# Kernel optimization log

Hardware: AMD Instinct MI355X
Metric: run time of the kernel (lower is better)

Reference implementation:

```python
import jax, jax.numpy as jnp
import numpy as np

N = 100000   # nodes
E = 1600000  # edges per view
B = 256      # graphs in batch
D = 128      # feature dim
H, C = 4, 32 # heads, per-head channels (H*C = 128)


def _seg_softmax(logits, seg, num_seg):
    # numerically stable softmax over segments (per-destination / per-graph)
    m = jax.ops.segment_max(logits, seg, num_segments=num_seg)
    e = jnp.exp(logits - m[seg])
    s = jax.ops.segment_sum(e, seg, num_segments=num_seg)
    return e / s[seg]


def _gat_conv(x, edge_index, W, att_src, att_dst, bias):
    # PyG GATConv with add_self_loops=True, concat heads
    n = x.shape[0]
    loop = jnp.arange(n, dtype=edge_index.dtype)
    src = jnp.concatenate([edge_index[0], loop])
    dst = jnp.concatenate([edge_index[1], loop])
    xh = (x @ W).reshape(n, H, C)                      # [N,H,C]
    a_src = jnp.einsum('nhc,hc->nh', xh, att_src)      # [N,H]
    a_dst = jnp.einsum('nhc,hc->nh', xh, att_dst)
    alpha = jax.nn.leaky_relu(a_src[src] + a_dst[dst], 0.2)   # [E+N,H]
    alpha = _seg_softmax(alpha, dst, n)
    msg = xh[src] * alpha[..., None]                   # [E+N,H,C]
    out = jax.ops.segment_sum(msg, dst, num_segments=n)
    return out.reshape(n, H * C) + bias


def _global_attention(h, batch, gate_W, gate_b):
    gate = (h @ gate_W + gate_b)[:, 0]                 # [N]
    a = _seg_softmax(gate, batch, B)
    return jax.ops.segment_sum(a[:, None] * h, batch, num_segments=B)  # [B,128]


def setup_inputs() -> dict:
    key = jax.random.key(0)
    ks = jax.random.split(key, 32)
    p = lambda k, shp: (jax.random.normal(k, shp, dtype=jnp.float32) * 0.05)
    inp = {
        'x': jax.random.normal(ks[0], (N, D), dtype=jnp.float32),
        'edge_index_ast': jax.random.randint(ks[1], (2, E), 0, N, dtype=jnp.int32),
        'edge_index_cfg': jax.random.randint(ks[2], (2, E), 0, N, dtype=jnp.int32),
        'edge_index_pdg': jax.random.randint(ks[3], (2, E), 0, N, dtype=jnp.int32),
        'batch': jnp.sort(jax.random.randint(ks[4], (N,), 0, B, dtype=jnp.int32)),
        'ln_g': jnp.ones((D,), jnp.float32),
        'ln_b': jnp.zeros((D,), jnp.float32),
        'proj_W': p(ks[5], (D, D)), 'proj_b': p(ks[6], (D,)),
        'W_ast': p(ks[7], (D, H * C)), 'att_src_ast': p(ks[8], (H, C)), 'att_dst_ast': p(ks[9], (H, C)), 'bias_ast': p(ks[10], (H * C,)),
        'W_cfg': p(ks[11], (D, H * C)), 'att_src_cfg': p(ks[12], (H, C)), 'att_dst_cfg': p(ks[13], (H, C)), 'bias_cfg': p(ks[14], (H * C,)),
        'W_pdg': p(ks[15], (D, H * C)), 'att_src_pdg': p(ks[16], (H, C)), 'att_dst_pdg': p(ks[17], (H, C)), 'bias_pdg': p(ks[18], (H * C,)),
        'gate_W': p(ks[19], (H * C, 1)), 'gate_b': p(ks[20], (1,)),
        'clf_W1': p(ks[21], (3 * H * C, 128)), 'clf_b1': p(ks[22], (128,)),
        'clf_W2': p(ks[23], (128, 1)), 'clf_b2': p(ks[24], (1,)),
    }
    return inp


def reference(x, edge_index_ast, edge_index_cfg, edge_index_pdg, batch,
              ln_g, ln_b, proj_W, proj_b,
              W_ast, att_src_ast, att_dst_ast, bias_ast,
              W_cfg, att_src_cfg, att_dst_cfg, bias_cfg,
              W_pdg, att_src_pdg, att_dst_pdg, bias_pdg,
              gate_W, gate_b, clf_W1, clf_b1, clf_W2, clf_b2):
    # LayerNorm + proj + LeakyReLU (dropout = eval/no-op)
    mu = jnp.mean(x, axis=-1, keepdims=True)
    var = jnp.var(x, axis=-1, keepdims=True)
    xn = (x - mu) * jax.lax.rsqrt(var + 1e-5) * ln_g + ln_b
    h0 = jax.nn.leaky_relu(xn @ proj_W + proj_b, 0.01)

    h_ast = jax.nn.elu(_gat_conv(h0, edge_index_ast, W_ast, att_src_ast, att_dst_ast, bias_ast))
    g_ast = _global_attention(h_ast, batch, gate_W, gate_b)
    h_cfg = jax.nn.elu(_gat_conv(h0, edge_index_cfg, W_cfg, att_src_cfg, att_dst_cfg, bias_cfg))
    g_cfg = _global_attention(h_cfg, batch, gate_W, gate_b)
    h_pdg = jax.nn.elu(_gat_conv(h0, edge_index_pdg, W_pdg, att_src_pdg, att_dst_pdg, bias_pdg))
    g_pdg = _global_attention(h_pdg, batch, gate_W, gate_b)

    combined = jnp.concatenate([g_ast, g_cfg, g_pdg], axis=1)  # [B, 384]
    hid = jax.nn.leaky_relu(combined @ clf_W1 + clf_b1, 0.01)
    return (hid @ clf_W2 + clf_b2).reshape(-1)                 # [B]
```

## Files before the change

kernel.cpp:

```cpp
#include <hip/hip_runtime.h>
#include <hip/hip_bf16.h>
#include <hip/hip_fp16.h>
#include <math.h>

#define NN 100000
#define EE 1600000
#define BB 256
#define DD 128
#define NBUCK 391
#define PBLK 384
#define CH 4167
#define TOTB (3 * PBLK)
#define ROWS_PAD 100096
#define EPV (EE + NN)

typedef short bf16x8 __attribute__((ext_vector_type(8)));
typedef float f32x4 __attribute__((ext_vector_type(4)));

__device__ __forceinline__ float bf2f(unsigned short u) {
    return __uint_as_float(((unsigned int)u) << 16);
}
__device__ __forceinline__ unsigned short f2bf(float f) {
    __hip_bfloat16 h = __float2bfloat16(f);
    return *(unsigned short*)&h;
}
__device__ __forceinline__ unsigned short f2h(float f) {
    __half h = __float2half(f);
    return *(unsigned short*)&h;
}
__device__ __forceinline__ float h2f(unsigned short u) {
    __half h = *(__half*)&u;
    return __half2float(h);
}

__global__ __launch_bounds__(256) void pack_wt(const float* __restrict__ W0,
                                               const float* __restrict__ W1,
                                               const float* __restrict__ W2,
                                               const float* __restrict__ W3,
                                               const float* __restrict__ ln_g,
                                               unsigned short* __restrict__ WT) {
    int which = blockIdx.y;
    const float* W = which == 0 ? W0 : which == 1 ? W1 : which == 2 ? W2 : W3;
    int i = blockIdx.x * 256 + threadIdx.x;
    int n = i >> 7, k = i & 127;
    float v = W[k * 128 + n];
    if (which == 0) v *= ln_g[k];
    WT[which * 16384 + i] = f2bf(v);
}

__global__ __launch_bounds__(128) void ln_consts(const float* __restrict__ W,
                                                 const float* __restrict__ g,
                                                 const float* __restrict__ b,
                                                 float* __restrict__ c12) {
    int n = threadIdx.x;
    float c1 = 0.f, c2 = 0.f;
    for (int k = 0; k < 128; k++) {
        float w = W[k * 128 + n];
        c1 = fmaf(g[k], w, c1);
        c2 = fmaf(b[k], w, c2);
    }
    c12[n] = c1;
    c12[128 + n] = c2;
}

__global__ __launch_bounds__(256) void gemm_proj(const float* __restrict__ X,
                                                 const unsigned short* __restrict__ WT,
                                                 const float* __restrict__ c12,
                                                 const float* __restrict__ pb,
                                                 unsigned short* __restrict__ Out) {
    int w = threadIdx.x >> 6, lane = threadIdx.x & 63;
    int ln = lane & 15, oct = lane >> 4;
    int row0 = blockIdx.x * 128 + w * 32;

    f32x4 acc[2][8];
    #pragma unroll
    for (int i = 0; i < 2; i++)
        #pragma unroll
        for (int j = 0; j < 8; j++) acc[i][j] = (f32x4){0.f, 0.f, 0.f, 0.f};

    const float* X0 = X + (size_t)(row0 + ln) * 128;
    const float* X1 = X + (size_t)(row0 + 16 + ln) * 128;
    const bf16x8* Wr = (const bf16x8*)(WT + (size_t)ln * 128);

    float s0 = 0.f, q0 = 0.f, s1 = 0.f, q1 = 0.f;
    #pragma unroll
    for (int kq = 0; kq < 4; kq++) {
        int koff = kq * 4 + oct;
        float4 xa = *(const float4*)(X0 + koff * 8);
        float4 xb = *(const float4*)(X0 + koff * 8 + 4);
        float4 ya = *(const float4*)(X1 + koff * 8);
        float4 yb = *(const float4*)(X1 + koff * 8 + 4);
        s0 += (xa.x + xa.y) + (xa.z + xa.w) + (xb.x + xb.y) + (xb.z + xb.w);
        q0 += xa.x * xa.x + xa.y * xa.y + xa.z * xa.z + xa.w * xa.w
            + xb.x * xb.x + xb.y * xb.y + xb.z * xb.z + xb.w * xb.w;
        s1 += (ya.x + ya.y) + (ya.z + ya.w) + (yb.x + yb.y) + (yb.z + yb.w);
        q1 += ya.x * ya.x + ya.y * ya.y + ya.z * ya.z + ya.w * ya.w
            + yb.x * yb.x + yb.y * yb.y + yb.z * yb.z + yb.w * yb.w;
        bf16x8 a0, a1;
        a0[0] = (short)f2bf(xa.x); a0[1] = (short)f2bf(xa.y); a0[2] = (short)f2bf(xa.z); a0[3] = (short)f2bf(xa.w);
        a0[4] = (short)f2bf(xb.x); a0[5] = (short)f2bf(xb.y); a0[6] = (short)f2bf(xb.z); a0[7] = (short)f2bf(xb.w);
        a1[0] = (short)f2bf(ya.x); a1[1] = (short)f2bf(ya.y); a1[2] = (short)f2bf(ya.z); a1[3] = (short)f2bf(ya.w);
        a1[4] = (short)f2bf(yb.x); a1[5] = (short)f2bf(yb.y); a1[6] = (short)f2bf(yb.z); a1[7] = (short)f2bf(yb.w);
        #pragma unroll
        for (int ct = 0; ct < 8; ct++) {
            bf16x8 bfr = Wr[ct * 16 * 16 + koff];
            acc[0][ct] = __builtin_amdgcn_mfma_f32_16x16x32_bf16(a0, bfr, acc[0][ct], 0, 0, 0);
            acc[1][ct] = __builtin_amdgcn_mfma_f32_16x16x32_bf16(a1, bfr, acc[1][ct], 0, 0, 0);
        }
    }
    #pragma unroll
    for (int m = 16; m < 64; m <<= 1) {
        s0 += __shfl_xor(s0, m); q0 += __shfl_xor(q0, m);
        s1 += __shfl_xor(s1, m); q1 += __shfl_xor(q1, m);
    }
    float mu0 = s0 * (1.0f / 128.0f);
    float rs0 = rsqrtf(q0 * (1.0f / 128.0f) - mu0 * mu0 + 1e-5f);
    float mu1 = s1 * (1.0f / 128.0f);
    float rs1 = rsqrtf(q1 * (1.0f / 128.0f) - mu1 * mu1 + 1e-5f);

    float c1v[8], c2v[8], pbv[8];
    #pragma unroll
    for (int ct = 0; ct < 8; ct++) {
        c1v[ct] = c12[ct * 16 + ln];
        c2v[ct] = c12[128 + ct * 16 + ln];
        pbv[ct] = pb[ct * 16 + ln];
    }

    #pragma unroll
    for (int rt = 0; rt < 2; rt++) {
        #pragma unroll
        for (int r = 0; r < 4; r++) {
            int src = oct * 4 + r;
            float rs_r = __shfl(rt ? rs1 : rs0, src);
            float mu_r = __shfl(rt ? mu1 : mu0, src);
            int row = row0 + rt * 16 + oct * 4 + r;
            #pragma unroll
            for (int ct = 0; ct < 8; ct++) {
                float v = rs_r * acc[rt][ct][r] - rs_r * mu_r * c1v[ct] + c2v[ct] + pbv[ct];
                v = v > 0.f ? v : 0.01f * v;
                Out[(size_t)row * 128 + ct * 16 + ln] = f2bf(v);
            }
        }
    }
}

__global__ __launch_bounds__(256) void gemm_view(const unsigned short* __restrict__ A,
                                                 const unsigned short* __restrict__ WT,
                                                 unsigned short* __restrict__ Out,
                                                 const float* __restrict__ asw,
                                                 const float* __restrict__ adw,
                                                 float* __restrict__ a_src,
                                                 float* __restrict__ a_dst) {
    int w = threadIdx.x >> 6, lane = threadIdx.x & 63;
    int ln = lane & 15, oct = lane >> 4;
    int row0 = blockIdx.x * 128 + w * 32;

    f32x4 acc[2][8];
    #pragma unroll
    for (int i = 0; i < 2; i++)
        #pragma unroll
        for (int j = 0; j < 8; j++) acc[i][j] = (f32x4){0.f, 0.f, 0.f, 0.f};

    const bf16x8* Ar0 = (const bf16x8*)(A + (size_t)(row0 + ln) * 128);
    const bf16x8* Ar1 = (const bf16x8*)(A + (size_t)(row0 + 16 + ln) * 128);
    const bf16x8* Wr  = (const bf16x8*)(WT + (size_t)ln * 128);

    #pragma unroll
    for (int kq = 0; kq < 4; kq++) {
        int koff = kq * 4 + oct;
        bf16x8 a0 = Ar0[koff];
        bf16x8 a1 = Ar1[koff];
        #pragma unroll
        for (int ct = 0; ct < 8; ct++) {
            bf16x8 bfr = Wr[ct * 16 * 16 + koff];
            acc[0][ct] = __builtin_amdgcn_mfma_f32_16x16x32_bf16(a0, bfr, acc[0][ct], 0, 0, 0);
            acc[1][ct] = __builtin_amdgcn_mfma_f32_16x16x32_bf16(a1, bfr, acc[1][ct], 0, 0, 0);
        }
    }

    float aswv[8], adwv[8];
    #pragma unroll
    for (int ct = 0; ct < 8; ct++) { aswv[ct] = asw[ct * 16 + ln]; adwv[ct] = adw[ct * 16 + ln]; }

    #pragma unroll
    for (int rt = 0; rt < 2; rt++) {
        #pragma unroll
        for (int r = 0; r < 4; r++) {
            int row = row0 + rt * 16 + oct * 4 + r;
            float sh_[4] = {0.f, 0.f, 0.f, 0.f}, dh_[4] = {0.f, 0.f, 0.f, 0.f};
            #pragma unroll
            for (int ct = 0; ct < 8; ct++) {
                float v = acc[rt][ct][r];
                Out[(size_t)row * 128 + ct * 16 + ln] = f2bf(v);
                sh_[ct >> 1] = fmaf(v, aswv[ct], sh_[ct >> 1]);
                dh_[ct >> 1] = fmaf(v, adwv[ct], dh_[ct >> 1]);
            }
            #pragma unroll
            for (int off = 1; off < 16; off <<= 1) {
                #pragma unroll
                for (int h = 0; h < 4; h++) {
                    sh_[h] += __shfl_xor(sh_[h], off);
                    dh_[h] += __shfl_xor(dh_[h], off);
                }
            }
            if (ln == 0) {
                *(float4*)(a_src + (size_t)row * 4) = make_float4(sh_[0], sh_[1], sh_[2], sh_[3]);
                *(float4*)(a_dst + (size_t)row * 4) = make_float4(dh_[0], dh_[1], dh_[2], dh_[3]);
            }
        }
    }
}

__global__ __launch_bounds__(256) void csr_hist(const int* __restrict__ e0,
                                                const int* __restrict__ e1,
                                                const int* __restrict__ e2,
                                                int* __restrict__ blockHistT) {
    int v = blockIdx.x / PBLK, p = blockIdx.x % PBLK;
    const int* ei = v == 0 ? e0 : v == 1 ? e1 : e2;
    __shared__ int h[NBUCK];
    for (int i = threadIdx.x; i < NBUCK; i += 256) h[i] = 0;
    __syncthreads();
    int ea = p * CH, ebnd = min(EE, ea + CH);
    int e = ea + threadIdx.x;
    for (; e + 768 < ebnd; e += 1024) {
        int d0 = ei[EE + e], d1 = ei[EE + e + 256];
        int d2 = ei[EE + e + 512], d3 = ei[EE + e + 768];
        atomicAdd(&h[((unsigned)d0) >> 8], 1);
        atomicAdd(&h[((unsigned)d1) >> 8], 1);
        atomicAdd(&h[((unsigned)d2) >> 8], 1);
        atomicAdd(&h[((unsigned)d3) >> 8], 1);
    }
    for (; e < ebnd; e += 256) atomicAdd(&h[((unsigned)ei[EE + e]) >> 8], 1);
    __syncthreads();
    for (int i = threadIdx.x; i < NBUCK; i += 256) blockHistT[i * TOTB + blockIdx.x] = h[i];
}

__global__ __launch_bounds__(256) void csr_bsum(const int* __restrict__ blockHistT,
                                                int* __restrict__ btot) {
    int wid = (blockIdx.x * 256 + threadIdx.x) >> 6;
    int lane = threadIdx.x & 63;
    if (wid >= 3 * NBUCK) return;
    int v = wid / NBUCK, b = wid - v * NBUCK;
    const int* row = blockHistT + (size_t)b * TOTB + v * PBLK;
    int s = 0;
    #pragma unroll
    for (int j = 0; j < 6; j++) s += row[lane * 6 + j];
    #pragma unroll
    for (int m = 1; m < 64; m <<= 1) s += __shfl_xor(s, m);
    if (lane == 0) btot[wid] = s;
}

__global__ __launch_bounds__(512) void csr_scan(const int* __restrict__ btot,
                                                int* __restrict__ ebstart,
                                                int* __restrict__ bstart) {
    int v = blockIdx.x, t = threadIdx.x;
    __shared__ int se[512], ss[512];
    int tot_e = (t < NBUCK) ? btot[v * NBUCK + t] : 0;
    int nval = (t < NBUCK) ? min(256, NN - t * 256) : 0;
    int tot_s = tot_e + nval;
    se[t] = tot_e; ss[t] = tot_s;
    __syncthreads();
    for (int s = 1; s < 512; s <<= 1) {
        int ae = (t >= s) ? se[t - s] : 0;
        int as_ = (t >= s) ? ss[t - s] : 0;
        __syncthreads();
        se[t] += ae; ss[t] += as_;
        __syncthreads();
    }
    if (t < NBUCK) {
        ebstart[v * (NBUCK + 1) + t] = se[t] - tot_e;
        bstart[v * (NBUCK + 1) + t] = ss[t] - tot_s;
    }
    if (t == NBUCK - 1) {
        ebstart[v * (NBUCK + 1) + NBUCK] = se[t];
        bstart[v * (NBUCK + 1) + NBUCK] = ss[t];
    }
}

__global__ __launch_bounds__(256) void csr_boff(const int* __restrict__ blockHistT,
                                                const int* __restrict__ ebstart,
                                                int* __restrict__ blockOffT) {
    int wid = (blockIdx.x * 256 + threadIdx.x) >> 6;
    int lane = threadIdx.x & 63;
    if (wid >= 3 * NBUCK) return;
    int v = wid / NBUCK, b = wid - v * NBUCK;
    const int* row = blockHistT + (size_t)b * TOTB + v * PBLK;
    int* orow = blockOffT + (size_t)b * TOTB + v * PBLK;
    int vals[6], lexcl[6];
    int ls = 0;
    #pragma unroll
    for (int j = 0; j < 6; j++) vals[j] = row[lane * 6 + j];
    #pragma unroll
    for (int j = 0; j < 6; j++) { lexcl[j] = ls; ls += vals[j]; }
    int incl = ls;
    #pragma unroll
    for (int m = 1; m < 64; m <<= 1) {
        int t = __shfl_up(incl, m);
        if (lane >= m) incl += t;
    }
    int wexcl = incl - ls;
    int base = ebstart[v * (NBUCK + 1) + b];
    #pragma unroll
    for (int j = 0; j < 6; j++) orow[lane * 6 + j] = base + wexcl + lexcl[j];
}

__global__ __launch_bounds__(256) void csr_scatter(const int* __restrict__ e0,
                                                   const int* __restrict__ e1,
                                                   const int* __restrict__ e2,
                                                   const int* __restrict__ blockOffT,
                                                   unsigned int* __restrict__ pairbuf) {
    int v = blockIdx.x / PBLK, p = blockIdx.x % PBLK;
    const int* ei = v == 0 ? e0 : v == 1 ? e1 : e2;
    __shared__ int cur[NBUCK];
    for (int i = threadIdx.x; i < NBUCK; i += 256) cur[i] = blockOffT[(size_t)i * TOTB + blockIdx.x];
    __syncthreads();
    int ea = p * CH, ebnd = min(EE, ea + CH);
    unsigned int* pb = pairbuf + (size_t)v * EE;
    int e = ea + threadIdx.x;
    for (; e + 768 < ebnd; e += 1024) {
        unsigned s0 = (unsigned)ei[e],       d0 = (unsigned)ei[EE + e];
        unsigned s1 = (unsigned)ei[e + 256], d1 = (unsigned)ei[EE + e + 256];
        unsigned s2 = (unsigned)ei[e + 512], d2 = (unsigned)ei[EE + e + 512];
        unsigned s3 = (unsigned)ei[e + 768], d3 = (unsigned)ei[EE + e + 768];
        int p0 = atomicAdd(&cur[d0 >> 8], 1);
        int p1 = atomicAdd(&cur[d1 >> 8], 1);
        int p2 = atomicAdd(&cur[d2 >> 8], 1);
        int p3 = atomicAdd(&cur[d3 >> 8], 1);
        pb[p0] = (s0 << 8) | (d0 & 255u);
        pb[p1] = (s1 << 8) | (d1 & 255u);
        pb[p2] = (s2 << 8) | (d2 & 255u);
        pb[p3] = (s3 << 8) | (d3 & 255u);
    }
    for (; e < ebnd; e += 256) {
        unsigned s = (unsigned)ei[e], d = (unsigned)ei[EE + e];
        int pos = atomicAdd(&cur[d >> 8], 1);
        pb[pos] = (s << 8) | (d & 255u);
    }
}

__global__ __launch_bounds__(256) void csr_fine(const unsigned int* __restrict__ pairbuf,
                                                const int* __restrict__ btot,
                                                const int* __restrict__ ebstart,
                                                const int* __restrict__ bstart,
                                                int* __restrict__ deg3,
                                                int* __restrict__ start3,
                                                unsigned int* __restrict__ ebuf3) {
    int v = blockIdx.x / NBUCK, b = blockIdx.x - v * NBUCK;
    int cnt   = btot[v * NBUCK + b];
    int pbase = ebstart[v * (NBUCK + 1) + b];
    int obase = bstart[v * (NBUCK + 1) + b];
    const unsigned int* pb = pairbuf + (size_t)v * EE + pbase;
    unsigned int* eb = ebuf3 + (size_t)v * EPV + obase;
    __shared__ int hist[256], scan[256], cur[256];
    int t = threadIdx.x;
    int node = b * 256 + t;
    int valid = (node < NN) ? 1 : 0;
    hist[t] = valid;
    __syncthreads();
    {
        int i = t;
        for (; i + 768 < cnt; i += 1024) {
            unsigned v0 = pb[i], v1 = pb[i + 256], v2 = pb[i + 512], v3 = pb[i + 768];
            atomicAdd(&hist[v0 & 255u], 1);
            atomicAdd(&hist[v1 & 255u], 1);
            atomicAdd(&hist[v2 & 255u], 1);
            atomicAdd(&hist[v3 & 255u], 1);
        }
        for (; i < cnt; i += 256) atomicAdd(&hist[pb[i] & 255u], 1);
    }
    __syncthreads();
    scan[t] = hist[t];
    __syncthreads();
    for (int s = 1; s < 256; s <<= 1) {
        int u = (t >= s) ? scan[t - s] : 0;
        __syncthreads();
        scan[t] += u;
        __syncthreads();
    }
    int excl = scan[t] - hist[t];
    cur[t] = excl + valid;
    if (valid) eb[excl] = (((unsigned)node) << 8) | ((unsigned)node & 255u);
    __syncthreads();
    {
        int i = t;
        for (; i + 768 < cnt; i += 1024) {
            unsigned v0 = pb[i], v1 = pb[i + 256], v2 = pb[i + 512], v3 = pb[i + 768];
            int p0 = atomicAdd(&cur[v0 & 255u], 1);
            int p1 = atomicAdd(&cur[v1 & 255u], 1);
            int p2 = atomicAdd(&cur[v2 & 255u], 1);
            int p3 = atomicAdd(&cur[v3 & 255u], 1);
            eb[p0] = v0; eb[p1] = v1; eb[p2] = v2; eb[p3] = v3;
        }
        for (; i < cnt; i += 256) {
            unsigned int val = pb[i];
            int pos = atomicAdd(&cur[val & 255u], 1);
            eb[pos] = val;
        }
    }
    if (valid) {
        deg3[v * NN + node] = hist[t];
        start3[v * NN + node] = obase + excl;
    }
}

__global__ __launch_bounds__(256) void aggregate_kernel(const unsigned short* __restrict__ xh,
                                                        const int* __restrict__ start,
                                                        const int* __restrict__ deg,
                                                        const unsigned int* __restrict__ ebuf,
                                                        const float* __restrict__ a_src,
                                                        const float* __restrict__ a_dst,
                                                        const float* __restrict__ bias,
                                                        const float* __restrict__ gw,
                                                        const float* __restrict__ gb,
                                                        unsigned short* __restrict__ hvb,
                                                        float* __restrict__ gexpv) {
    int node = (blockIdx.x * 256 + threadIdx.x) >> 6;
    int lane = threadIdx.x & 63;
    if (node >= NN) return;
    int h = lane >> 4;
    int st = start[node];
    int cnt = deg[node];
    const char* xb = (const char*)xh;
    int laneoff = lane * 4;
    float4 ad4 = *(const float4*)(a_dst + (size_t)node * 4);

    float accx = 0.f, accy = 0.f, den = 0.f;
    for (int j0 = 0; j0 < cnt; j0 += 64) {
        int nj = min(64, cnt - j0);
        int src_l = 0;
        unsigned u01 = 0, u23 = 0;
        if (lane < nj) {
            src_l = (int)(ebuf[st + j0 + lane] >> 8);
            float4 as4 = *(const float4*)(a_src + (size_t)src_l * 4);
            float t0 = as4.x + ad4.x, t1 = as4.y + ad4.y;
            float t2 = as4.z + ad4.z, t3 = as4.w + ad4.w;
            t0 = fmaxf(t0, 0.f) + 0.2f * fminf(t0, 0.f);
            t1 = fmaxf(t1, 0.f) + 0.2f * fminf(t1, 0.f);
            t2 = fmaxf(t2, 0.f) + 0.2f * fminf(t2, 0.f);
            t3 = fmaxf(t3, 0.f) + 0.2f * fminf(t3, 0.f);
            u01 = (unsigned)f2h(exp2f(t0 * 1.442695041f)) |
                  ((unsigned)f2h(exp2f(t1 * 1.442695041f)) << 16);
            u23 = (unsigned)f2h(exp2f(t2 * 1.442695041f)) |
                  ((unsigned)f2h(exp2f(t3 * 1.442695041f)) << 16);
        }
        int jj = 0;
        for (; jj + 4 <= nj; jj += 4) {
            int s0 = __builtin_amdgcn_readlane(src_l, jj);
            int s1 = __builtin_amdgcn_readlane(src_l, jj + 1);
            int s2 = __builtin_amdgcn_readlane(src_l, jj + 2);
            int s3 = __builtin_amdgcn_readlane(src_l, jj + 3);
            unsigned pa0 = (unsigned)__builtin_amdgcn_readlane((int)u01, jj);
            unsigned pb0 = (unsigned)__builtin_amdgcn_readlane((int)u23, jj);
            unsigned pa1 = (unsigned)__builtin_amdgcn_readlane((int)u01, jj + 1);
            unsigned pb1 = (unsigned)__builtin_amdgcn_readlane((int)u23, jj + 1);
            unsigned pa2 = (unsigned)__builtin_amdgcn_readlane((int)u01, jj + 2);
            unsigned pb2 = (unsigned)__builtin_amdgcn_readlane((int)u23, jj + 2);
            unsigned pa3 = (unsigned)__builtin_amdgcn_readlane((int)u01, jj + 3);
            unsigned pb3 = (unsigned)__builtin_amdgcn_readlane((int)u23, jj + 3);
            unsigned k0 = (h < 2) ? pa0 : pb0;
            unsigned k1 = (h < 2) ? pa1 : pb1;
            unsigned k2 = (h < 2) ? pa2 : pb2;
            unsigned k3 = (h < 2) ? pa3 : pb3;
            float w0 = h2f((unsigned short)((h & 1) ? (k0 >> 16) : (k0 & 0xffffu)));
            float w1 = h2f((unsigned short)((h & 1) ? (k1 >> 16) : (k1 & 0xffffu)));
            float w2 = h2f((unsigned short)((h & 1) ? (k2 >> 16) : (k2 & 0xffffu)));
            float w3 = h2f((unsigned short)((h & 1) ? (k3 >> 16) : (k3 & 0xffffu)));
            unsigned int x0 = *(const unsigned int*)(xb + (((size_t)(unsigned)s0) << 8) + laneoff);
            unsigned int x1 = *(const unsigned int*)(xb + (((size_t)(unsigned)s1) << 8) + laneoff);
            unsigned int x2 = *(const unsigned int*)(xb + (((size_t)(unsigned)s2) << 8) + laneoff);
            unsigned int x3 = *(const unsigned int*)(xb + (((size_t)(unsigned)s3) << 8) + laneoff);
            den += (w0 + w1) + (w2 + w3);
            accx = fmaf(w0, __uint_as_float(x0 << 16), accx);
            accy = fmaf(w0, __uint_as_float(x0 & 0xffff0000u), accy);
            accx = fmaf(w1, __uint_as_float(x1 << 16), accx);
            accy = fmaf(w1, __uint_as_float(x1 & 0xffff0000u), accy);
            accx = fmaf(w2, __uint_as_float(x2 << 16), accx);
            accy = fmaf(w2, __uint_as_float(x2 & 0xffff0000u), accy);
            accx = fmaf(w3, __uint_as_float(x3 << 16), accx);
            accy = fmaf(w3, __uint_as_float(x3 & 0xffff0000u), accy);
        }
        for (; jj < nj; jj++) {
            int s = __builtin_amdgcn_readlane(src_l, jj);
            unsigned pa = (unsigned)__builtin_amdgcn_readlane((int)u01, jj);
            unsigned pbk = (unsigned)__builtin_amdgcn_readlane((int)u23, jj);
            unsigned k = (h < 2) ? pa : pbk;
            float w = h2f((unsigned short)((h & 1) ? (k >> 16) : (k & 0xffffu)));
            unsigned int xv = *(const unsigned int*)(xb + (((size_t)(unsigned)s) << 8) + laneoff);
            den += w;
            accx = fmaf(w, __uint_as_float(xv << 16), accx);
            accy = fmaf(w, __uint_as_float(xv & 0xffff0000u), accy);
        }
    }
    float inv = 1.0f / den;
    float2 bb = *(const float2*)(bias + lane * 2);
    float o0 = accx * inv + bb.x;
    float o1 = accy * inv + bb.y;
    o0 = o0 > 0.f ? o0 : exp2f(o0 * 1.442695041f) - 1.0f;
    o1 = o1 > 0.f ? o1 : exp2f(o1 * 1.442695041f) - 1.0f;
    unsigned int packed = (unsigned)f2bf(o0) | ((unsigned)f2bf(o1) << 16);
    *(unsigned int*)(hvb + (size_t)node * 128 + lane * 2) = packed;
    float2 g2 = *(const float2*)(gw + lane * 2);
    float gp = o0 * g2.x + o1 * g2.y;
    #pragma unroll
    for (int m = 1; m < 64; m <<= 1) gp += __shfl_xor(gp, m);
    if (lane == 0) gexpv[node] = exp2f((gp + gb[0]) * 1.442695041f);
}

__global__ __launch_bounds__(1024) void pool_kernel(const unsigned short* __restrict__ hvb,
                                                    const float* __restrict__ gexpv,
                                                    const int* __restrict__ batch,
                                                    float* __restrict__ gout,
                                                    int voff) {
    int b = blockIdx.x;
    int g = threadIdx.x >> 7;
    int ch = threadIdx.x & 127;
    int l = 0, r = NN;
    while (l < r) { int m = (l + r) >> 1; if (batch[m] < b) l = m + 1; else r = m; }
    int s0 = l;
    r = NN;
    while (l < r) { int m = (l + r) >> 1; if (batch[m] < b + 1) l = m + 1; else r = m; }
    int s1 = l;
    float acc = 0.f, wsum = 0.f;
    for (int n = s0 + g; n < s1; n += 8) {
        float w = gexpv[n];
        wsum += w;
        acc = fmaf(w, bf2f(hvb[(size_t)n * 128 + ch]), acc);
    }
    __shared__ float sacc[8][128];
    __shared__ float sws[8];
    sacc[g][ch] = acc;
    if (ch == 0) sws[g] = wsum;
    __syncthreads();
    if (g == 0) {
        float a = 0.f, w = 0.f;
        #pragma unroll
        for (int i = 0; i < 8; i++) { a += sacc[i][ch]; w += sws[i]; }
        gout[b * 384 + voff + ch] = (s1 > s0) ? a / w : 0.f;
    }
}

__global__ __launch_bounds__(128) void clf_kernel(const float* __restrict__ gout,
                                                  const float* __restrict__ W1,
                                                  const float* __restrict__ b1,
                                                  const float* __restrict__ W2,
                                                  const float* __restrict__ b2,
                                                  float* __restrict__ out) {
    int b = blockIdx.x;
    int j = threadIdx.x;
    float acc = b1[j];
    for (int k = 0; k < 384; k++) acc = fmaf(gout[b * 384 + k], W1[k * 128 + j], acc);
    acc = acc > 0.f ? acc : 0.01f * acc;
    float p = acc * W2[j];
    #pragma unroll
    for (int m = 1; m < 64; m <<= 1) p += __shfl_xor(p, m);
    __shared__ float sh[2];
    if ((j & 63) == 0) sh[j >> 6] = p;
    __syncthreads();
    if (j == 0) out[b] = sh[0] + sh[1] + b2[0];
}

extern "C" void kernel_launch(void* const* d_in, const int* in_sizes, int n_in,
                              void* d_out, int out_size, void* d_ws, size_t ws_size,
                              hipStream_t stream) {
    const float* x      = (const float*)d_in[0];
    const int*   ei[3]  = {(const int*)d_in[1], (const int*)d_in[2], (const int*)d_in[3]};
    const int*   batch  = (const int*)d_in[4];
    const float* ln_g   = (const float*)d_in[5];
    const float* ln_b   = (const float*)d_in[6];
    const float* proj_W = (const float*)d_in[7];
    const float* proj_b = (const float*)d_in[8];
    const float* Wv[3]  = {(const float*)d_in[9],  (const float*)d_in[13], (const float*)d_in[17]};
    const float* asv[3] = {(const float*)d_in[10], (const float*)d_in[14], (const float*)d_in[18]};
    const float* adv[3] = {(const float*)d_in[11], (const float*)d_in[15], (const float*)d_in[19]};
    const float* bv[3]  = {(const float*)d_in[12], (const float*)d_in[16], (const float*)d_in[20]};
    const float* gate_W = (const float*)d_in[21];
    const float* gate_b = (const float*)d_in[22];
    const float* clf_W1 = (const float*)d_in[23];
    const float* clf_b1 = (const float*)d_in[24];
    const float* clf_W2 = (const float*)d_in[25];
    const float* clf_b2 = (const float*)d_in[26];
    float* out = (float*)d_out;

    (void)in_sizes; (void)n_in; (void)out_size; (void)ws_size;

    char* base = (char*)d_ws;
    size_t off = 0;
    auto nxt = [&](size_t bytes) { char* r = base + off; off += (bytes + 255) & ~(size_t)255; return r; };
    unsigned short* h0   = (unsigned short*)nxt((size_t)ROWS_PAD * 128 * 2);
    unsigned short* xh   = (unsigned short*)nxt((size_t)ROWS_PAD * 128 * 2);
    unsigned short* hvb  = (unsigned short*)nxt((size_t)NN * 128 * 2);
    unsigned short* WT   = (unsigned short*)nxt(4 * 16384 * 2);
    float* c12    = (float*)nxt(256 * 4);
    float* a_src  = (float*)nxt((size_t)ROWS_PAD * 4 * 4);
    float* a_dst  = (float*)nxt((size_t)ROWS_PAD * 4 * 4);
    float* gexpv  = (float*)nxt(NN * 4);
    float* gout   = (float*)nxt(BB * 384 * 4);
    int* deg3     = (int*)nxt(3 * NN * 4);
    int* start3   = (int*)nxt(3 * NN * 4);
    unsigned int* ebuf3 = (unsigned int*)nxt(((size_t)3 * EPV + 64) * 4);
    int* btot     = (int*)nxt(3 * NBUCK * 4);
    int* ebstart  = (int*)nxt(3 * (NBUCK + 1) * 4);
    int* bstart   = (int*)nxt(3 * (NBUCK + 1) * 4);
    int* blockHistT = (int*)nxt((size_t)NBUCK * TOTB * 4);
    int* blockOffT  = (int*)nxt((size_t)NBUCK * TOTB * 4);
    unsigned int* pairbuf = (unsigned int*)nxt((size_t)3 * EE * 4);

    pack_wt<<<dim3(64, 4), 256, 0, stream>>>(proj_W, Wv[0], Wv[1], Wv[2], ln_g, WT);
    ln_consts<<<1, 128, 0, stream>>>(proj_W, ln_g, ln_b, c12);
    csr_hist<<<TOTB, 256, 0, stream>>>(ei[0], ei[1], ei[2], blockHistT);
    csr_bsum<<<(3 * NBUCK + 3) / 4, 256, 0, stream>>>(blockHistT, btot);
    csr_scan<<<3, 512, 0, stream>>>(btot, ebstart, bstart);
    csr_boff<<<(3 * NBUCK + 3) / 4, 256, 0, stream>>>(blockHistT, ebstart, blockOffT);
    csr_scatter<<<TOTB, 256, 0, stream>>>(ei[0], ei[1], ei[2], blockOffT, pairbuf);
    csr_fine<<<3 * NBUCK, 256, 0, stream>>>(pairbuf, btot, ebstart, bstart, deg3, start3, ebuf3);
    gemm_proj<<<782, 256, 0, stream>>>(x, WT, c12, proj_b, h0);
    for (int v = 0; v < 3; v++) {
        gemm_view<<<782, 256, 0, stream>>>(h0, WT + (1 + v) * 16384, xh,
                                           asv[v], adv[v], a_src, a_dst);
        aggregate_kernel<<<25000, 256, 0, stream>>>(xh, start3 + v * NN, deg3 + v * NN,
                                                    ebuf3 + (size_t)v * EPV,
                                                    a_src, a_dst,
                                                    bv[v], gate_W, gate_b, hvb, gexpv);
        pool_kernel<<<256, 1024, 0, stream>>>(hvb, gexpv, batch, gout, v * 128);
    }
    clf_kernel<<<256, 128, 0, stream>>>(gout, clf_W1, clf_b1, clf_W2, clf_b2, out);
}
```

Measured before the change: 710.2 us.

## Fuse CSR build kernels with projection GEMMs and switch features to fp16

```diff
diff --git a/kernel.cpp b/kernel.cpp
--- a/kernel.cpp
+++ b/kernel.cpp
@@ -6,20 +6,17 @@
 #define NN 100000
 #define EE 1600000
 #define BB 256
-#define DD 128
 #define NBUCK 391
 #define PBLK 384
 #define CH 4167
 #define TOTB (3 * PBLK)
 #define ROWS_PAD 100096
 #define EPV (EE + NN)
+#define LOG2E 1.442695041f
 
 typedef short bf16x8 __attribute__((ext_vector_type(8)));
 typedef float f32x4 __attribute__((ext_vector_type(4)));
 
-__device__ __forceinline__ float bf2f(unsigned short u) {
-    return __uint_as_float(((unsigned int)u) << 16);
-}
 __device__ __forceinline__ unsigned short f2bf(float f) {
     __hip_bfloat16 h = __float2bfloat16(f);
     return *(unsigned short*)&h;
@@ -63,14 +60,41 @@
     c12[128 + n] = c2;
 }
 
-__global__ __launch_bounds__(256) void gemm_proj(const float* __restrict__ X,
-                                                 const unsigned short* __restrict__ WT,
-                                                 const float* __restrict__ c12,
-                                                 const float* __restrict__ pb,
-                                                 unsigned short* __restrict__ Out) {
-    int w = threadIdx.x >> 6, lane = threadIdx.x & 63;
+
+__device__ __forceinline__ void hist_body(int bid, int tid,
+                                          const int* __restrict__ e0,
+                                          const int* __restrict__ e1,
+                                          const int* __restrict__ e2,
+                                          int* __restrict__ blockHistT) {
+    int v = bid / PBLK, p = bid % PBLK;
+    const int* ei = v == 0 ? e0 : v == 1 ? e1 : e2;
+    __shared__ int h[NBUCK];
+    for (int i = tid; i < NBUCK; i += 256) h[i] = 0;
+    __syncthreads();
+    int ea = p * CH, ebnd = min(EE, ea + CH);
+    int e = ea + tid;
+    for (; e + 768 < ebnd; e += 1024) {
+        int d0 = ei[EE + e], d1 = ei[EE + e + 256];
+        int d2 = ei[EE + e + 512], d3 = ei[EE + e + 768];
+        atomicAdd(&h[((unsigned)d0) >> 8], 1);
+        atomicAdd(&h[((unsigned)d1) >> 8], 1);
+        atomicAdd(&h[((unsigned)d2) >> 8], 1);
+        atomicAdd(&h[((unsigned)d3) >> 8], 1);
+    }
+    for (; e < ebnd; e += 256) atomicAdd(&h[((unsigned)ei[EE + e]) >> 8], 1);
+    __syncthreads();
+    for (int i = tid; i < NBUCK; i += 256) blockHistT[i * TOTB + bid] = h[i];
+}
+
+__device__ __forceinline__ void proj_body(int nb, int tid,
+                                          const float* __restrict__ X,
+                                          const unsigned short* __restrict__ WT,
+                                          const float* __restrict__ c12,
+                                          const float* __restrict__ pb,
+                                          unsigned short* __restrict__ Out) {
+    int w = tid >> 6, lane = tid & 63;
     int ln = lane & 15, oct = lane >> 4;
-    int row0 = blockIdx.x * 128 + w * 32;
+    int row0 = nb * 128 + w * 32;
 
     f32x4 acc[2][8];
     #pragma unroll
@@ -78,8 +102,8 @@
         #pragma unroll
         for (int j = 0; j < 8; j++) acc[i][j] = (f32x4){0.f, 0.f, 0.f, 0.f};
 
-    const float* X0 = X + (size_t)(row0 + ln) * 128;
-    const float* X1 = X + (size_t)(row0 + 16 + ln) * 128;
+    const float* X0 = X + (size_t)min(row0 + ln, NN - 1) * 128;
+    const float* X1 = X + (size_t)min(row0 + 16 + ln, NN - 1) * 128;
     const bf16x8* Wr = (const bf16x8*)(WT + (size_t)ln * 128);
 
     float s0 = 0.f, q0 = 0.f, s1 = 0.f, q1 = 0.f;
@@ -125,7 +149,6 @@
         c2v[ct] = c12[128 + ct * 16 + ln];
         pbv[ct] = pb[ct * 16 + ln];
     }
-
     #pragma unroll
     for (int rt = 0; rt < 2; rt++) {
         #pragma unroll
@@ -144,16 +167,52 @@
     }
 }
 
-__global__ __launch_bounds__(256) void gemm_view(const unsigned short* __restrict__ A,
-                                                 const unsigned short* __restrict__ WT,
-                                                 unsigned short* __restrict__ Out,
-                                                 const float* __restrict__ asw,
-                                                 const float* __restrict__ adw,
-                                                 float* __restrict__ a_src,
-                                                 float* __restrict__ a_dst) {
-    int w = threadIdx.x >> 6, lane = threadIdx.x & 63;
+__device__ __forceinline__ void scatter_body(int bid, int tid,
+                                             const int* __restrict__ e0,
+                                             const int* __restrict__ e1,
+                                             const int* __restrict__ e2,
+                                             const int* __restrict__ blockOffT,
+                                             unsigned int* __restrict__ pairbuf) {
+    int v = bid / PBLK, p = bid % PBLK;
+    const int* ei = v == 0 ? e0 : v == 1 ? e1 : e2;
+    __shared__ int cur[NBUCK];
+    for (int i = tid; i < NBUCK; i += 256) cur[i] = blockOffT[(size_t)i * TOTB + bid];
+    __syncthreads();
+    int ea = p * CH, ebnd = min(EE, ea + CH);
+    unsigned int* pbuf = pairbuf + (size_t)v * EE;
+    int e = ea + tid;
+    for (; e + 768 < ebnd; e += 1024) {
+        unsigned s0 = (unsigned)ei[e],       d0 = (unsigned)ei[EE + e];
+        unsigned s1 = (unsigned)ei[e + 256], d1 = (unsigned)ei[EE + e + 256];
+        unsigned s2 = (unsigned)ei[e + 512], d2 = (unsigned)ei[EE + e + 512];
+        unsigned s3 = (unsigned)ei[e + 768], d3 = (unsigned)ei[EE + e + 768];
+        int p0 = atomicAdd(&cur[d0 >> 8], 1);
+        int p1 = atomicAdd(&cur[d1 >> 8], 1);
+        int p2 = atomicAdd(&cur[d2 >> 8], 1);
+        int p3 = atomicAdd(&cur[d3 >> 8], 1);
+        pbuf[p0] = (s0 << 8) | (d0 & 255u);
+        pbuf[p1] = (s1 << 8) | (d1 & 255u);
+        pbuf[p2] = (s2 << 8) | (d2 & 255u);
+        pbuf[p3] = (s3 << 8) | (d3 & 255u);
+    }
+    for (; e < ebnd; e += 256) {
+        unsigned s = (unsigned)ei[e], d = (unsigned)ei[EE + e];
+        int pos = atomicAdd(&cur[d >> 8], 1);
+        pbuf[pos] = (s << 8) | (d & 255u);
+    }
+}
+
+__device__ __forceinline__ void view_body(int nb, int tid,
+                                          const unsigned short* __restrict__ h0,
+                                          const unsigned short* __restrict__ WTv,
+                                          const float* __restrict__ asw,
+                                          const float* __restrict__ adw,
+                                          unsigned short* __restrict__ Out,
+                                          float* __restrict__ a_src,
+                                          float* __restrict__ a_dst) {
+    int w = tid >> 6, lane = tid & 63;
     int ln = lane & 15, oct = lane >> 4;
-    int row0 = blockIdx.x * 128 + w * 32;
+    int row0 = nb * 128 + w * 32;
 
     f32x4 acc[2][8];
     #pragma unroll
@@ -161,9 +220,9 @@
         #pragma unroll
         for (int j = 0; j < 8; j++) acc[i][j] = (f32x4){0.f, 0.f, 0.f, 0.f};
 
-    const bf16x8* Ar0 = (const bf16x8*)(A + (size_t)(row0 + ln) * 128);
-    const bf16x8* Ar1 = (const bf16x8*)(A + (size_t)(row0 + 16 + ln) * 128);
-    const bf16x8* Wr  = (const bf16x8*)(WT + (size_t)ln * 128);
+    const bf16x8* Ar0 = (const bf16x8*)(h0 + (size_t)(row0 + ln) * 128);
+    const bf16x8* Ar1 = (const bf16x8*)(h0 + (size_t)(row0 + 16 + ln) * 128);
+    const bf16x8* Wr  = (const bf16x8*)(WTv + (size_t)ln * 128);
 
     #pragma unroll
     for (int kq = 0; kq < 4; kq++) {
@@ -177,7 +236,6 @@
             acc[1][ct] = __builtin_amdgcn_mfma_f32_16x16x32_bf16(a1, bfr, acc[1][ct], 0, 0, 0);
         }
     }
-
     float aswv[8], adwv[8];
     #pragma unroll
     for (int ct = 0; ct < 8; ct++) { aswv[ct] = asw[ct * 16 + ln]; adwv[ct] = adw[ct * 16 + ln]; }
@@ -190,10 +248,10 @@
             float sh_[4] = {0.f, 0.f, 0.f, 0.f}, dh_[4] = {0.f, 0.f, 0.f, 0.f};
             #pragma unroll
             for (int ct = 0; ct < 8; ct++) {
-                float v = acc[rt][ct][r];
-                Out[(size_t)row * 128 + ct * 16 + ln] = f2bf(v);
-                sh_[ct >> 1] = fmaf(v, aswv[ct], sh_[ct >> 1]);
-                dh_[ct >> 1] = fmaf(v, adwv[ct], dh_[ct >> 1]);
+                float vv = acc[rt][ct][r];
+                Out[(size_t)row * 128 + ct * 16 + ln] = f2h(vv);
+                sh_[ct >> 1] = fmaf(vv, aswv[ct], sh_[ct >> 1]);
+                dh_[ct >> 1] = fmaf(vv, adwv[ct], dh_[ct >> 1]);
             }
             #pragma unroll
             for (int off = 1; off < 16; off <<= 1) {
@@ -211,28 +269,32 @@
     }
 }
 
-__global__ __launch_bounds__(256) void csr_hist(const int* __restrict__ e0,
-                                                const int* __restrict__ e1,
-                                                const int* __restrict__ e2,
-                                                int* __restrict__ blockHistT) {
-    int v = blockIdx.x / PBLK, p = blockIdx.x % PBLK;
-    const int* ei = v == 0 ? e0 : v == 1 ? e1 : e2;
-    __shared__ int h[NBUCK];
-    for (int i = threadIdx.x; i < NBUCK; i += 256) h[i] = 0;
-    __syncthreads();
-    int ea = p * CH, ebnd = min(EE, ea + CH);
-    int e = ea + threadIdx.x;
-    for (; e + 768 < ebnd; e += 1024) {
-        int d0 = ei[EE + e], d1 = ei[EE + e + 256];
-        int d2 = ei[EE + e + 512], d3 = ei[EE + e + 768];
-        atomicAdd(&h[((unsigned)d0) >> 8], 1);
-        atomicAdd(&h[((unsigned)d1) >> 8], 1);
-        atomicAdd(&h[((unsigned)d2) >> 8], 1);
-        atomicAdd(&h[((unsigned)d3) >> 8], 1);
-    }
-    for (; e < ebnd; e += 256) atomicAdd(&h[((unsigned)ei[EE + e]) >> 8], 1);
-    __syncthreads();
-    for (int i = threadIdx.x; i < NBUCK; i += 256) blockHistT[i * TOTB + blockIdx.x] = h[i];
+__global__ __launch_bounds__(256) void fat_hist_proj(const int* e0, const int* e1, const int* e2,
+                                                     int* blockHistT,
+                                                     const float* X, const unsigned short* WT,
+                                                     const float* c12, const float* pb,
+                                                     unsigned short* h0) {
+    if (blockIdx.x < TOTB) hist_body(blockIdx.x, threadIdx.x, e0, e1, e2, blockHistT);
+    else proj_body(blockIdx.x - TOTB, threadIdx.x, X, WT, c12, pb, h0);
+}
+
+__global__ __launch_bounds__(256) void fat_scatter_view(const int* e0, const int* e1, const int* e2,
+                                                        const int* blockOffT, unsigned int* pairbuf,
+                                                        const unsigned short* h0, const unsigned short* WT,
+                                                        const float* as0, const float* ad0,
+                                                        unsigned short* xh, float* a_src, float* a_dst) {
+    if (blockIdx.x < TOTB) scatter_body(blockIdx.x, threadIdx.x, e0, e1, e2, blockOffT, pairbuf);
+    else view_body(blockIdx.x - TOTB, threadIdx.x, h0, WT + 16384, as0, ad0, xh, a_src, a_dst);
+}
+
+__global__ __launch_bounds__(256) void gemm_view(const unsigned short* __restrict__ h0,
+                                                 const unsigned short* __restrict__ WTv,
+                                                 const float* __restrict__ asw,
+                                                 const float* __restrict__ adw,
+                                                 unsigned short* __restrict__ Out,
+                                                 float* __restrict__ a_src,
+                                                 float* __restrict__ a_dst) {
+    view_body(blockIdx.x, threadIdx.x, h0, WTv, asw, adw, Out, a_src, a_dst);
 }
 
 __global__ __launch_bounds__(256) void csr_bsum(const int* __restrict__ blockHistT,
@@ -302,40 +364,6 @@
     int base = ebstart[v * (NBUCK + 1) + b];
     #pragma unroll
     for (int j = 0; j < 6; j++) orow[lane * 6 + j] = base + wexcl + lexcl[j];
-}
-
-__global__ __launch_bounds__(256) void csr_scatter(const int* __restrict__ e0,
-                                                   const int* __restrict__ e1,
-                                                   const int* __restrict__ e2,
-                                                   const int* __restrict__ blockOffT,
-                                                   unsigned int* __restrict__ pairbuf) {
-    int v = blockIdx.x / PBLK, p = blockIdx.x % PBLK;
-    const int* ei = v == 0 ? e0 : v == 1 ? e1 : e2;
-    __shared__ int cur[NBUCK];
-    for (int i = threadIdx.x; i < NBUCK; i += 256) cur[i] = blockOffT[(size_t)i * TOTB + blockIdx.x];
-    __syncthreads();
-    int ea = p * CH, ebnd = min(EE, ea + CH);
-    unsigned int* pb = pairbuf + (size_t)v * EE;
-    int e = ea + threadIdx.x;
-    for (; e + 768 < ebnd; e += 1024) {
-        unsigned s0 = (unsigned)ei[e],       d0 = (unsigned)ei[EE + e];
-        unsigned s1 = (unsigned)ei[e + 256], d1 = (unsigned)ei[EE + e + 256];
-        unsigned s2 = (unsigned)ei[e + 512], d2 = (unsigned)ei[EE + e + 512];
-        unsigned s3 = (unsigned)ei[e + 768], d3 = (unsigned)ei[EE + e + 768];
-        int p0 = atomicAdd(&cur[d0 >> 8], 1);
-        int p1 = atomicAdd(&cur[d1 >> 8], 1);
-        int p2 = atomicAdd(&cur[d2 >> 8], 1);
-        int p3 = atomicAdd(&cur[d3 >> 8], 1);
-        pb[p0] = (s0 << 8) | (d0 & 255u);
-        pb[p1] = (s1 << 8) | (d1 & 255u);
-        pb[p2] = (s2 << 8) | (d2 & 255u);
-        pb[p3] = (s3 << 8) | (d3 & 255u);
-    }
-    for (; e < ebnd; e += 256) {
-        unsigned s = (unsigned)ei[e], d = (unsigned)ei[EE + e];
-        int pos = atomicAdd(&cur[d >> 8], 1);
-        pb[pos] = (s << 8) | (d & 255u);
-    }
 }
 
 __global__ __launch_bounds__(256) void csr_fine(const unsigned int* __restrict__ pairbuf,
@@ -423,8 +451,11 @@
     const char* xb = (const char*)xh;
     int laneoff = lane * 4;
     float4 ad4 = *(const float4*)(a_dst + (size_t)node * 4);
-
-    float accx = 0.f, accy = 0.f, den = 0.f;
+    int shamt = (h & 1) * 16;
+    bool lowpair = (h < 2);
+
+    float accx = 0.f, accy = 0.f;
+    float d0s = 0.f, d1s = 0.f, d2s = 0.f, d3s = 0.f;
     for (int j0 = 0; j0 < cnt; j0 += 64) {
         int nj = min(64, cnt - j0);
         int src_l = 0;
@@ -438,10 +469,14 @@
             t1 = fmaxf(t1, 0.f) + 0.2f * fminf(t1, 0.f);
             t2 = fmaxf(t2, 0.f) + 0.2f * fminf(t2, 0.f);
             t3 = fmaxf(t3, 0.f) + 0.2f * fminf(t3, 0.f);
-            u01 = (unsigned)f2h(exp2f(t0 * 1.442695041f)) |
-                  ((unsigned)f2h(exp2f(t1 * 1.442695041f)) << 16);
-            u23 = (unsigned)f2h(exp2f(t2 * 1.442695041f)) |
-                  ((unsigned)f2h(exp2f(t3 * 1.442695041f)) << 16);
+            unsigned short w0h = f2h(exp2f(t0 * LOG2E));
+            unsigned short w1h = f2h(exp2f(t1 * LOG2E));
+            unsigned short w2h = f2h(exp2f(t2 * LOG2E));
+            unsigned short w3h = f2h(exp2f(t3 * LOG2E));
+            d0s += h2f(w0h); d1s += h2f(w1h);
+            d2s += h2f(w2h); d3s += h2f(w3h);
+            u01 = (unsigned)w0h | ((unsigned)w1h << 16);
+            u23 = (unsigned)w2h | ((unsigned)w3h << 16);
         }
         int jj = 0;
         for (; jj + 4 <= nj; jj += 4) {
@@ -449,61 +484,67 @@
             int s1 = __builtin_amdgcn_readlane(src_l, jj + 1);
             int s2 = __builtin_amdgcn_readlane(src_l, jj + 2);
             int s3 = __builtin_amdgcn_readlane(src_l, jj + 3);
-            unsigned pa0 = (unsigned)__builtin_amdgcn_readlane((int)u01, jj);
-            unsigned pb0 = (unsigned)__builtin_amdgcn_readlane((int)u23, jj);
-            unsigned pa1 = (unsigned)__builtin_amdgcn_readlane((int)u01, jj + 1);
-            unsigned pb1 = (unsigned)__builtin_amdgcn_readlane((int)u23, jj + 1);
-            unsigned pa2 = (unsigned)__builtin_amdgcn_readlane((int)u01, jj + 2);
-            unsigned pb2 = (unsigned)__builtin_amdgcn_readlane((int)u23, jj + 2);
-            unsigned pa3 = (unsigned)__builtin_amdgcn_readlane((int)u01, jj + 3);
-            unsigned pb3 = (unsigned)__builtin_amdgcn_readlane((int)u23, jj + 3);
-            unsigned k0 = (h < 2) ? pa0 : pb0;
-            unsigned k1 = (h < 2) ? pa1 : pb1;
-            unsigned k2 = (h < 2) ? pa2 : pb2;
-            unsigned k3 = (h < 2) ? pa3 : pb3;
-            float w0 = h2f((unsigned short)((h & 1) ? (k0 >> 16) : (k0 & 0xffffu)));
-            float w1 = h2f((unsigned short)((h & 1) ? (k1 >> 16) : (k1 & 0xffffu)));
-            float w2 = h2f((unsigned short)((h & 1) ? (k2 >> 16) : (k2 & 0xffffu)));
-            float w3 = h2f((unsigned short)((h & 1) ? (k3 >> 16) : (k3 & 0xffffu)));
-            unsigned int x0 = *(const unsigned int*)(xb + (((size_t)(unsigned)s0) << 8) + laneoff);
-            unsigned int x1 = *(const unsigned int*)(xb + (((size_t)(unsigned)s1) << 8) + laneoff);
-            unsigned int x2 = *(const unsigned int*)(xb + (((size_t)(unsigned)s2) << 8) + laneoff);
-            unsigned int x3 = *(const unsigned int*)(xb + (((size_t)(unsigned)s3) << 8) + laneoff);
-            den += (w0 + w1) + (w2 + w3);
-            accx = fmaf(w0, __uint_as_float(x0 << 16), accx);
-            accy = fmaf(w0, __uint_as_float(x0 & 0xffff0000u), accy);
-            accx = fmaf(w1, __uint_as_float(x1 << 16), accx);
-            accy = fmaf(w1, __uint_as_float(x1 & 0xffff0000u), accy);
-            accx = fmaf(w2, __uint_as_float(x2 << 16), accx);
-            accy = fmaf(w2, __uint_as_float(x2 & 0xffff0000u), accy);
-            accx = fmaf(w3, __uint_as_float(x3 << 16), accx);
-            accy = fmaf(w3, __uint_as_float(x3 & 0xffff0000u), accy);
+            unsigned a0 = (unsigned)__builtin_amdgcn_readlane((int)u01, jj);
+            unsigned b0 = (unsigned)__builtin_amdgcn_readlane((int)u23, jj);
+            unsigned a1 = (unsigned)__builtin_amdgcn_readlane((int)u01, jj + 1);
+            unsigned b1 = (unsigned)__builtin_amdgcn_readlane((int)u23, jj + 1);
+            unsigned a2 = (unsigned)__builtin_amdgcn_readlane((int)u01, jj + 2);
+            unsigned b2 = (unsigned)__builtin_amdgcn_readlane((int)u23, jj + 2);
+            unsigned a3 = (unsigned)__builtin_amdgcn_readlane((int)u01, jj + 3);
+            unsigned b3 = (unsigned)__builtin_amdgcn_readlane((int)u23, jj + 3);
+            unsigned k0 = lowpair ? a0 : b0;
+            unsigned k1 = lowpair ? a1 : b1;
+            unsigned k2 = lowpair ? a2 : b2;
+            unsigned k3 = lowpair ? a3 : b3;
+            __half2 x0 = *(const __half2*)(xb + (((size_t)(unsigned)s0) << 8) + laneoff);
+            __half2 x1 = *(const __half2*)(xb + (((size_t)(unsigned)s1) << 8) + laneoff);
+            __half2 x2 = *(const __half2*)(xb + (((size_t)(unsigned)s2) << 8) + laneoff);
+            __half2 x3 = *(const __half2*)(xb + (((size_t)(unsigned)s3) << 8) + laneoff);
+            float w0 = h2f((unsigned short)(k0 >> shamt));
+            float w1 = h2f((unsigned short)(k1 >> shamt));
+            float w2 = h2f((unsigned short)(k2 >> shamt));
+            float w3 = h2f((unsigned short)(k3 >> shamt));
+            accx = fmaf(__low2float(x0), w0, accx);
+            accy = fmaf(__high2float(x0), w0, accy);
+            accx = fmaf(__low2float(x1), w1, accx);
+            accy = fmaf(__high2float(x1), w1, accy);
+            accx = fmaf(__low2float(x2), w2, accx);
+            accy = fmaf(__high2float(x2), w2, accy);
+            accx = fmaf(__low2float(x3), w3, accx);
+            accy = fmaf(__high2float(x3), w3, accy);
         }
         for (; jj < nj; jj++) {
             int s = __builtin_amdgcn_readlane(src_l, jj);
-            unsigned pa = (unsigned)__builtin_amdgcn_readlane((int)u01, jj);
-            unsigned pbk = (unsigned)__builtin_amdgcn_readlane((int)u23, jj);
-            unsigned k = (h < 2) ? pa : pbk;
-            float w = h2f((unsigned short)((h & 1) ? (k >> 16) : (k & 0xffffu)));
-            unsigned int xv = *(const unsigned int*)(xb + (((size_t)(unsigned)s) << 8) + laneoff);
-            den += w;
-            accx = fmaf(w, __uint_as_float(xv << 16), accx);
-            accy = fmaf(w, __uint_as_float(xv & 0xffff0000u), accy);
-        }
-    }
+            unsigned a = (unsigned)__builtin_amdgcn_readlane((int)u01, jj);
+            unsigned bq = (unsigned)__builtin_amdgcn_readlane((int)u23, jj);
+            unsigned k = lowpair ? a : bq;
+            float w = h2f((unsigned short)(k >> shamt));
+            __half2 xv = *(const __half2*)(xb + (((size_t)(unsigned)s) << 8) + laneoff);
+            accx = fmaf(__low2float(xv), w, accx);
+            accy = fmaf(__high2float(xv), w, accy);
+        }
+    }
+    #pragma unroll
+    for (int m = 1; m < 64; m <<= 1) {
+        d0s += __shfl_xor(d0s, m);
+        d1s += __shfl_xor(d1s, m);
+        d2s += __shfl_xor(d2s, m);
+        d3s += __shfl_xor(d3s, m);
+    }
+    float den = (h == 0) ? d0s : (h == 1) ? d1s : (h == 2) ? d2s : d3s;
     float inv = 1.0f / den;
     float2 bb = *(const float2*)(bias + lane * 2);
     float o0 = accx * inv + bb.x;
     float o1 = accy * inv + bb.y;
-    o0 = o0 > 0.f ? o0 : exp2f(o0 * 1.442695041f) - 1.0f;
-    o1 = o1 > 0.f ? o1 : exp2f(o1 * 1.442695041f) - 1.0f;
-    unsigned int packed = (unsigned)f2bf(o0) | ((unsigned)f2bf(o1) << 16);
+    o0 = o0 > 0.f ? o0 : exp2f(o0 * LOG2E) - 1.0f;
+    o1 = o1 > 0.f ? o1 : exp2f(o1 * LOG2E) - 1.0f;
+    unsigned int packed = (unsigned)f2h(o0) | ((unsigned)f2h(o1) << 16);
     *(unsigned int*)(hvb + (size_t)node * 128 + lane * 2) = packed;
     float2 g2 = *(const float2*)(gw + lane * 2);
     float gp = o0 * g2.x + o1 * g2.y;
     #pragma unroll
     for (int m = 1; m < 64; m <<= 1) gp += __shfl_xor(gp, m);
-    if (lane == 0) gexpv[node] = exp2f((gp + gb[0]) * 1.442695041f);
+    if (lane == 0) gexpv[node] = exp2f((gp + gb[0]) * LOG2E);
 }
 
 __global__ __launch_bounds__(1024) void pool_kernel(const unsigned short* __restrict__ hvb,
@@ -524,7 +565,7 @@
     for (int n = s0 + g; n < s1; n += 8) {
         float w = gexpv[n];
         wsum += w;
-        acc = fmaf(w, bf2f(hvb[(size_t)n * 128 + ch]), acc);
+        acc = fmaf(w, h2f(hvb[(size_t)n * 128 + ch]), acc);
     }
     __shared__ float sacc[8][128];
     __shared__ float sws[8];
@@ -607,16 +648,18 @@
 
     pack_wt<<<dim3(64, 4), 256, 0, stream>>>(proj_W, Wv[0], Wv[1], Wv[2], ln_g, WT);
     ln_consts<<<1, 128, 0, stream>>>(proj_W, ln_g, ln_b, c12);
-    csr_hist<<<TOTB, 256, 0, stream>>>(ei[0], ei[1], ei[2], blockHistT);
+    fat_hist_proj<<<TOTB + 782, 256, 0, stream>>>(ei[0], ei[1], ei[2], blockHistT,
+                                                  x, WT, c12, proj_b, h0);
     csr_bsum<<<(3 * NBUCK + 3) / 4, 256, 0, stream>>>(blockHistT, btot);
     csr_scan<<<3, 512, 0, stream>>>(btot, ebstart, bstart);
     csr_boff<<<(3 * NBUCK + 3) / 4, 256, 0, stream>>>(blockHistT, ebstart, blockOffT);
-    csr_scatter<<<TOTB, 256, 0, stream>>>(ei[0], ei[1], ei[2], blockOffT, pairbuf);
+    fat_scatter_view<<<TOTB + 782, 256, 0, stream>>>(ei[0], ei[1], ei[2], blockOffT, pairbuf,
+                                                     h0, WT, asv[0], adv[0], xh, a_src, a_dst);
     csr_fine<<<3 * NBUCK, 256, 0, stream>>>(pairbuf, btot, ebstart, bstart, deg3, start3, ebuf3);
-    gemm_proj<<<782, 256, 0, stream>>>(x, WT, c12, proj_b, h0);
     for (int v = 0; v < 3; v++) {
-        gemm_view<<<782, 256, 0, stream>>>(h0, WT + (1 + v) * 16384, xh,
-                                           asv[v], adv[v], a_src, a_dst);
+        if (v > 0)
+            gemm_view<<<782, 256, 0, stream>>>(h0, WT + (size_t)(1 + v) * 16384,
+                                               asv[v], adv[v], xh, a_src, a_dst);
         aggregate_kernel<<<25000, 256, 0, stream>>>(xh, start3 + v * NN, deg3 + v * NN,
                                                     ebuf3 + (size_t)v * EPV,
                                                     a_src, a_dst,
```

Measured after the change: 696.1 us. 1.02x faster.
